# Performance work log

Hardware: AMD Instinct MI355X
Metric: run time of the kernel (lower is better)

The kernel has to match this reference:

```python
import jax, jax.numpy as jnp
import numpy as np

FFT_LENGTH = 2048
HOP_LENGTH = 512  # window_length // 4, window_length == fft_length


def _hann_periodic(n):
    # tf.signal.hann_window(n, periodic=True)
    return (0.5 - 0.5 * jnp.cos(2.0 * jnp.pi * jnp.arange(n) / n)).astype(jnp.float32)


def setup_inputs() -> dict:
    key = jax.random.key(0)
    k1, k2 = jax.random.split(key)
    B, F, NB = 4, 4000, FFT_LENGTH // 2 + 1
    spec_real = jax.random.normal(k1, (B, F, NB), dtype=jnp.float32)
    spec_imag = jax.random.normal(k2, (B, F, NB), dtype=jnp.float32)
    return {"spec_real": spec_real, "spec_imag": spec_imag}


def reference(spec_real, spec_imag) -> jnp.ndarray:
    fft_length, hop = FFT_LENGTH, HOP_LENGTH
    B, F, _ = spec_real.shape
    window = _hann_periodic(fft_length)  # [N], window_length == fft_length so no padding

    # irfft of the complex spectrogram -> time-domain frames [B, F, N]
    frames = jnp.fft.irfft(spec_real + 1j * spec_imag, n=fft_length).astype(jnp.float32)
    windowed = window * frames  # [B, F, N]

    # overlap-and-add: output length L = (F-1)*hop + N
    L = (F - 1) * hop + fft_length
    idx = (jnp.arange(F) * hop)[:, None] + jnp.arange(fft_length)[None, :]  # [F, N]
    out = jnp.zeros((B, L), jnp.float32).at[:, idx].add(windowed)

    # librosa window_sumsquare: overlap-add of squared window, guard tiny values
    wsq = jnp.zeros((L,), jnp.float32).at[idx].add(window * window)
    tiny = jnp.float32(np.finfo(np.float32).tiny)
    window_sum = jnp.where(wsq > tiny, wsq, jnp.float32(1.0))

    y = out / window_sum
    # center=True: trim fft_length//2 on each side
    half = fft_length // 2
    return y[:, half:L - half]
```

## Files before the change

### kernel.cpp

```cpp
#include <hip/hip_runtime.h>
#include <math.h>

#define NB       1025
#define M        1024
#define FFTN     2048
#define HOP      512
#define NFRAMES  4000
#define BATCH    4
#define OUT_T    2047488
#define R_HOPS   8
#define NPAIR    251
#define PI_F     3.14159265358979323846f

__device__ __forceinline__ float2 cmul(float2 a, float2 b) {
    return make_float2(a.x*b.x - a.y*b.y, a.x*b.y + a.y*b.x);
}
__device__ __forceinline__ float4 cmul4(float4 v, float2 w) {
    return make_float4(v.x*w.x - v.y*w.y, v.x*w.y + v.y*w.x,
                       v.z*w.x - v.w*w.y, v.z*w.y + v.w*w.x);
}
__device__ __forceinline__ float4 f4add(float4 a, float4 b){ return make_float4(a.x+b.x, a.y+b.y, a.z+b.z, a.w+b.w); }
__device__ __forceinline__ float4 f4sub(float4 a, float4 b){ return make_float4(a.x-b.x, a.y-b.y, a.z-b.z, a.w-b.w); }
__device__ __forceinline__ float4 f4addi(float4 a, float4 b){ return make_float4(a.x-b.y, a.y+b.x, a.z-b.w, a.w+b.z); }
__device__ __forceinline__ float4 f4subi(float4 a, float4 b){ return make_float4(a.x+b.y, a.y-b.x, a.z+b.w, a.w-b.z); }

__device__ __forceinline__ int SW4(int i) { return i ^ ((i >> 3) & 7); }

__device__ __forceinline__ float wsq_at(int p) {
    int u  = p + FFTN / 2;
    int fm = u >> 9;
    int n0 = u & 511;
    float wsq = 0.f;
    #pragma unroll
    for (int jj = 0; jj < 4; ++jj) {
        int fr = fm - jj;
        if (fr >= 0 && fr < NFRAMES) {
            int n = n0 + (jj << 9);
            float sw = __sinf((PI_F / (float)FFTN) * (float)n);
            float w  = sw * sw;
            wsq += w * w;
        }
    }
    const float tiny = 1.17549435e-38f;
    return (wsq > tiny) ? wsq : 1.0f;
}
__device__ __forceinline__ float invw_at(int p, bool edge) {
    if (edge && (p < 512 || p >= OUT_T - 512)) return 1.0f / wsq_at(p);
    return (2.0f / 3.0f);
}

template<int ST>
__device__ __forceinline__ void stage4x(const float4* __restrict__ src,
                                        float4* __restrict__ dst, int j, float2 w1) {
    const int Ns = 1 << (2 * ST);
    float4 v0 = src[SW4(j)];
    float4 v1 = src[SW4(j + 256)];
    float4 v2 = src[SW4(j + 512)];
    float4 v3 = src[SW4(j + 768)];
    float2 w2 = cmul(w1, w1);
    float2 w3 = cmul(w2, w1);
    v1 = cmul4(v1, w1); v2 = cmul4(v2, w2); v3 = cmul4(v3, w3);
    float4 t0 = f4add(v0, v2), t1 = f4sub(v0, v2);
    float4 t2 = f4add(v1, v3), t3 = f4sub(v1, v3);
    int jm = j & (Ns - 1);
    int idxD = ((j >> (2 * ST)) << (2 * ST + 2)) + jm;
    dst[SW4(idxD         )] = f4add(t0, t2);
    dst[SW4(idxD +     Ns)] = f4addi(t1, t3);
    dst[SW4(idxD + 2 * Ns)] = f4sub(t0, t2);
    dst[SW4(idxD + 3 * Ns)] = f4subi(t1, t3);
}

__device__ __forceinline__ void load_spec(const float* __restrict__ sr,
                                          const float* __restrict__ si,
                                          int b, int f, int j,
                                          float* car, float* cai,
                                          float* cbr, float* cbi) {
    const size_t fb = ((size_t)b * NFRAMES + f) * NB;
    const float* __restrict__ xr = sr + fb;
    const float* __restrict__ xi = si + fb;
    #pragma unroll
    for (int kk = 0; kk < 4; ++kk) {
        int k  = j + kk * 256;
        int mk = M - k;
        car[kk] = xr[k];  cai[kk] = xi[k];
        cbr[kk] = xr[mk]; cbi[kk] = xi[mk];
    }
}

__device__ __forceinline__ void pack2_st0(float4* __restrict__ dst, int j,
                                          const float2* twp,
                                          const float* a1r, const float* a1i,
                                          const float* b1r, const float* b1i,
                                          const float* a2r, const float* a2i,
                                          const float* b2r, const float* b2i) {
    float4 z[4];
    #pragma unroll
    for (int kk = 0; kk < 4; ++kk) {
        float ar = a1r[kk], ai = a1i[kk], br = b1r[kk], bi = b1i[kk];
        float cr = a2r[kk], ci = a2i[kk], dr = b2r[kk], di = b2i[kk];
        if (kk == 0 && j == 0) { ai = 0.f; bi = 0.f; ci = 0.f; di = 0.f; }
        float2 t = twp[kk];
        float Er = 0.5f*(ar+br), Ei = 0.5f*(ai-bi), Dr = 0.5f*(ar-br), Di = 0.5f*(ai+bi);
        float Or = Dr*t.x - Di*t.y, Oi = Dr*t.y + Di*t.x;
        float Fr = 0.5f*(cr+dr), Fi = 0.5f*(ci-di), Gr = 0.5f*(cr-dr), Gi = 0.5f*(ci+di);
        float Pr = Gr*t.x - Gi*t.y, Pi = Gr*t.y + Gi*t.x;
        z[kk] = make_float4(Er - Oi, Ei + Or, Fr - Pi, Fi + Pr);
    }
    float4 t0 = f4add(z[0], z[2]), t1 = f4sub(z[0], z[2]);
    float4 t2 = f4add(z[1], z[3]), t3 = f4sub(z[1], z[3]);
    dst[SW4(4*j    )] = f4add(t0, t2);
    dst[SW4(4*j + 1)] = f4addi(t1, t3);
    dst[SW4(4*j + 2)] = f4sub(t0, t2);
    dst[SW4(4*j + 3)] = f4subi(t1, t3);
}

__global__ __launch_bounds__(256) void istft_pair_kernel(
    const float* __restrict__ sr, const float* __restrict__ si,
    float* __restrict__ out)
{
    __shared__ float4 buf0[M];
    __shared__ float4 buf1[M];

    const int blk  = blockIdx.x;
    const int b    = blk / NPAIR;
    const int pr   = blk - b * NPAIR;
    const int regA = 2 * pr;
    const int s0hA = regA * R_HOPS;
    const int s0hB = s0hA + R_HOPS;
    const int j    = threadIdx.x;
    const bool edgeA = (regA == 0) || (regA == 500);
    const bool edgeB = (regA + 1 == 500);

    float2 tw_pack[4];
    #pragma unroll
    for (int kk = 0; kk < 4; ++kk) {
        int k = j + kk * 256;
        float s, c;
        __sincosf(PI_F * (float)k * (1.0f / (float)M), &s, &c);
        tw_pack[kk] = make_float2(c, s);
    }
    float2 w1s[4];
    #pragma unroll
    for (int st = 1; st <= 4; ++st) {
        int Ns = 1 << (2 * st);
        int jm = j & (Ns - 1);
        float ang = (0.5f * PI_F / (float)Ns) * (float)jm;
        float s1, c1;
        __sincosf(ang, &s1, &c1);
        w1s[st-1] = make_float2(c1, s1);
    }
    float wreg[4][2];
    #pragma unroll
    for (int q = 0; q < 4; ++q) {
        int n = j + q * 256;
        #pragma unroll
        for (int h = 0; h < 2; ++h) {
            int t = 2 * n + h;
            float swv = __sinf((PI_F / (float)FFTN) * (float)t);
            wreg[q][h] = swv * swv * (1.0f / 1024.0f);
        }
    }

    float2 AccA[R_HOPS], AccB[R_HOPS];
    #pragma unroll
    for (int s = 0; s < R_HOPS; ++s) {
        AccA[s] = make_float2(0.f, 0.f);
        AccB[s] = make_float2(0.f, 0.f);
    }

    #pragma unroll
    for (int it = 0; it < 11; ++it) {
        const int fA = s0hA - 3 + it;
        const int fB = s0hB - 3 + it;
        const bool vA = (fA >= 0) && (fA < NFRAMES);
        const bool vB = (fB >= 0) && (fB < NFRAMES);
        if (!vA && !vB) continue;

        int fAc = fA < 0 ? 0 : (fA > NFRAMES-1 ? NFRAMES-1 : fA);
        int fBc = fB < 0 ? 0 : (fB > NFRAMES-1 ? NFRAMES-1 : fB);

        float a1r[4], a1i[4], b1r[4], b1i[4];
        float a2r[4], a2i[4], b2r[4], b2i[4];
        load_spec(sr, si, b, fAc, j, a1r, a1i, b1r, b1i);
        load_spec(sr, si, b, fBc, j, a2r, a2i, b2r, b2i);

        pack2_st0(buf0, j, tw_pack, a1r, a1i, b1r, b1i, a2r, a2i, b2r, b2i);
        __syncthreads();
        stage4x<1>(buf0, buf1, j, w1s[0]);
        __syncthreads();
        stage4x<2>(buf1, buf0, j, w1s[1]);
        __syncthreads();
        stage4x<3>(buf0, buf1, j, w1s[2]);
        __syncthreads();

        {
            float4 v0 = buf1[SW4(j)];
            float4 v1 = buf1[SW4(j + 256)];
            float4 v2 = buf1[SW4(j + 512)];
            float4 v3 = buf1[SW4(j + 768)];
            float2 w1 = w1s[3];
            float2 w2 = cmul(w1, w1);
            float2 w3 = cmul(w2, w1);
            v1 = cmul4(v1, w1); v2 = cmul4(v2, w2); v3 = cmul4(v3, w3);
            float4 t0 = f4add(v0, v2), t1 = f4sub(v0, v2);
            float4 t2 = f4add(v1, v3), t3 = f4sub(v1, v3);
            float4 g[4];
            g[0] = f4add(t0, t2);
            g[1] = f4addi(t1, t3);
            g[2] = f4sub(t0, t2);
            g[3] = f4subi(t1, t3);
            if (vA) {
                #pragma unroll
                for (int q = 0; q < 4; ++q) {
                    const int s = it - 3 + q;
                    if (s >= 0 && s < R_HOPS) {
                        AccA[s].x += g[q].x * wreg[q][0];
                        AccA[s].y += g[q].y * wreg[q][1];
                    }
                }
            }
            if (vB) {
                #pragma unroll
                for (int q = 0; q < 4; ++q) {
                    const int s = it - 3 + q;
                    if (s >= 0 && s < R_HOPS) {
                        AccB[s].x += g[q].z * wreg[q][0];
                        AccB[s].y += g[q].w * wreg[q][1];
                    }
                }
            }
        }
        __syncthreads();
    }

    float* outb = out + (size_t)b * OUT_T;
    {
        const int base_u = s0hA * HOP;
        #pragma unroll
        for (int s = 0; s < R_HOPS; ++s) {
            int i2 = j + 256 * s;
            int p0 = base_u + 2 * i2 - FFTN / 2;
            int p1 = p0 + 1;
            if ((unsigned)p0 < (unsigned)OUT_T) outb[p0] = AccA[s].x * invw_at(p0, edgeA);
            if ((unsigned)p1 < (unsigned)OUT_T) outb[p1] = AccA[s].y * invw_at(p1, edgeA);
        }
    }
    {
        const int base_u = s0hB * HOP;
        #pragma unroll
        for (int s = 0; s < R_HOPS; ++s) {
            int i2 = j + 256 * s;
            int p0 = base_u + 2 * i2 - FFTN / 2;
            int p1 = p0 + 1;
            if ((unsigned)p0 < (unsigned)OUT_T) outb[p0] = AccB[s].x * invw_at(p0, edgeB);
            if ((unsigned)p1 < (unsigned)OUT_T) outb[p1] = AccB[s].y * invw_at(p1, edgeB);
        }
    }
}

extern "C" void kernel_launch(void* const* d_in, const int* in_sizes, int n_in,
                              void* d_out, int out_size, void* d_ws, size_t ws_size,
                              hipStream_t stream) {
    const float* sr = (const float*)d_in[0];
    const float* si = (const float*)d_in[1];
    float* out = (float*)d_out;
    istft_pair_kernel<<<BATCH * NPAIR, 256, 0, stream>>>(sr, si, out);
}
```

Baseline: 53.92 us.

## Prefetch next frame spectrum into registers while FFT stages run

Loads for the next frame pair's spectrum are issued before the shared-memory FFT stages of the current frame run, so global-memory latency overlaps LDS work. The trailing barrier at the end of each iteration is dropped, since the next iteration's writes to buf0 happen only after every thread has passed the barrier following stage 3. In exchange, 32 extra floats of live registers per thread can lower occupancy, and out-of-range frames are now loaded (clamped) rather than skipped.

```diff
diff --git a/kernel.cpp b/kernel.cpp
--- a/kernel.cpp
+++ b/kernel.cpp
@@ -168,32 +168,44 @@
         AccB[s] = make_float2(0.f, 0.f);
     }
 
+    float a1r[4], a1i[4], b1r[4], b1i[4];
+    float a2r[4], a2i[4], b2r[4], b2i[4];
+    {
+        int fA0 = s0hA - 3; fA0 = fA0 < 0 ? 0 : (fA0 > NFRAMES-1 ? NFRAMES-1 : fA0);
+        int fB0 = s0hB - 3; fB0 = fB0 < 0 ? 0 : (fB0 > NFRAMES-1 ? NFRAMES-1 : fB0);
+        load_spec(sr, si, b, fA0, j, a1r, a1i, b1r, b1i);
+        load_spec(sr, si, b, fB0, j, a2r, a2i, b2r, b2i);
+    }
+
     #pragma unroll
     for (int it = 0; it < 11; ++it) {
         const int fA = s0hA - 3 + it;
         const int fB = s0hB - 3 + it;
         const bool vA = (fA >= 0) && (fA < NFRAMES);
         const bool vB = (fB >= 0) && (fB < NFRAMES);
-        if (!vA && !vB) continue;
-
-        int fAc = fA < 0 ? 0 : (fA > NFRAMES-1 ? NFRAMES-1 : fA);
-        int fBc = fB < 0 ? 0 : (fB > NFRAMES-1 ? NFRAMES-1 : fB);
-
-        float a1r[4], a1i[4], b1r[4], b1i[4];
-        float a2r[4], a2i[4], b2r[4], b2i[4];
-        load_spec(sr, si, b, fAc, j, a1r, a1i, b1r, b1i);
-        load_spec(sr, si, b, fBc, j, a2r, a2i, b2r, b2i);
-
-        pack2_st0(buf0, j, tw_pack, a1r, a1i, b1r, b1i, a2r, a2i, b2r, b2i);
-        __syncthreads();
-        stage4x<1>(buf0, buf1, j, w1s[0]);
-        __syncthreads();
-        stage4x<2>(buf1, buf0, j, w1s[1]);
-        __syncthreads();
-        stage4x<3>(buf0, buf1, j, w1s[2]);
-        __syncthreads();
-
-        {
+
+        if (vA || vB) {
+            pack2_st0(buf0, j, tw_pack, a1r, a1i, b1r, b1i, a2r, a2i, b2r, b2i);
+        }
+
+        float n1r[4], n1i[4], m1r[4], m1i[4];
+        float n2r[4], n2i[4], m2r[4], m2i[4];
+        if (it < 10) {
+            int fAn = fA + 1; fAn = fAn < 0 ? 0 : (fAn > NFRAMES-1 ? NFRAMES-1 : fAn);
+            int fBn = fB + 1; fBn = fBn < 0 ? 0 : (fBn > NFRAMES-1 ? NFRAMES-1 : fBn);
+            load_spec(sr, si, b, fAn, j, n1r, n1i, m1r, m1i);
+            load_spec(sr, si, b, fBn, j, n2r, n2i, m2r, m2i);
+        }
+
+        if (vA || vB) {
+            __syncthreads();
+            stage4x<1>(buf0, buf1, j, w1s[0]);
+            __syncthreads();
+            stage4x<2>(buf1, buf0, j, w1s[1]);
+            __syncthreads();
+            stage4x<3>(buf0, buf1, j, w1s[2]);
+            __syncthreads();
+
             float4 v0 = buf1[SW4(j)];
             float4 v1 = buf1[SW4(j + 256)];
             float4 v2 = buf1[SW4(j + 512)];
@@ -230,7 +242,16 @@
                 }
             }
         }
-        __syncthreads();
+
+        if (it < 10) {
+            #pragma unroll
+            for (int kk = 0; kk < 4; ++kk) {
+                a1r[kk] = n1r[kk]; a1i[kk] = n1i[kk];
+                b1r[kk] = m1r[kk]; b1i[kk] = m1i[kk];
+                a2r[kk] = n2r[kk]; a2i[kk] = n2i[kk];
+                b2r[kk] = m2r[kk]; b2i[kk] = m2i[kk];
+            }
+        }
     }
 
     float* outb = out + (size_t)b * OUT_T;
```

Measured after the change: 60.68 us. 1.13x slower.
